# Kernel tuning notes

Hardware: AMD Instinct MI355X
Metric: run time of the kernel (lower is better)

The kernel has to match this reference:

```python
import math
import jax, jax.numpy as jnp
import numpy as np

# dims (from init_kwargs / forward signature)
B, N, K = 8, 1024, 8            # batch, nodes, num_neighbors
NC, TED, TEC = 64, 128, 64      # num_channels, time_embedding_dim, time_embedding_channels
C = NC + TEC                    # model dim = 128
H, Dh = 8, 16                   # heads, dim_head
HD = H * Dh
L = 4                           # num_layers
RH = 32                         # radial-net hidden width
NPATH = 10                      # radial scalars: k00,k10,k01,k11a,k11b,v00,v10,v01,v11a,v11b


def _g(k, shape, fan_in):
    return jax.random.normal(k, shape, dtype=jnp.float32) / np.sqrt(float(fan_in))


def setup_inputs() -> dict:
    key = jax.random.key(0)
    ks = jax.random.split(key, 16)
    return dict(
        x=jax.random.normal(ks[0], (B, N, 3), dtype=jnp.float32),
        y=jax.random.normal(ks[1], (B, N, 3), dtype=jnp.float32),
        t=jax.random.uniform(ks[2], (B,), dtype=jnp.float32) * 1000.0,
        Wt1=_g(ks[3], (TED, TED), TED), bt1=jnp.zeros((TED,), jnp.float32),
        Wt2=_g(ks[4], (TED, TEC), TED), bt2=jnp.zeros((TEC,), jnp.float32),
        Win0=_g(ks[5], (TEC + 3, C), TEC + 3), bin0=jnp.zeros((C,), jnp.float32),
        Win1=_g(ks[6], (1, C), 1),
        Wqkv=_g(ks[7], (L, 12, C, HD), C),           # q0,q1,k00,k10,k01,k11a,k11b,v00,v10,v01,v11a,v11b
        Wr1=_g(ks[8], (L, 1, RH), 1), br1=jnp.zeros((L, RH), jnp.float32),
        Wr2=_g(ks[9], (L, RH, H * NPATH), RH), br2=jnp.zeros((L, H * NPATH), jnp.float32),
        Wo=_g(ks[10], (L, 2, HD, C), HD), bo=jnp.zeros((L, 2, C), jnp.float32),
        Wout=_g(ks[11], (3, C), C), bout=jnp.zeros((3,), jnp.float32),
    )


def _forward(x, y, t, Wt1, bt1, Wt2, bt2, Win0, bin0, Win1, Wqkv,
             Wr1, br1, Wr2, br2, Wo, bo, Wout, bout):
    b, n = x.shape[0], x.shape[1]
    # sinusoidal time embedding + time MLP
    half = TED // 2
    freqs = jnp.exp(-math.log(10000.0) * jnp.arange(half, dtype=x.dtype) / half)
    emb = t[:, None] * freqs
    temb = jnp.concatenate([jnp.sin(emb), jnp.cos(emb)], axis=-1)          # [B,TED]
    temb = jax.nn.silu(temb @ Wt1 + bt1) @ Wt2 + bt2                        # [B,TEC]

    # degree-0 input = [time_embed | coords], degree-1 input = coords (1 channel)
    deg0 = jnp.concatenate([jnp.broadcast_to(temb[:, None, :], (b, n, TEC)), x], axis=-1)
    f0 = deg0 @ Win0 + bin0                                                 # [B,N,C]
    f1 = jnp.einsum('bnv,c->bncv', x, Win1[0])                              # [B,N,C,3]

    # k-nearest-neighbor graph on coordinates (shared across layers)
    d2 = jnp.sum((x[:, :, None, :] - x[:, None, :, :]) ** 2, axis=-1)       # [B,N,N]
    d2 = d2 + jnp.eye(n, dtype=x.dtype) * 1e9                               # exclude self
    _, idx = jax.lax.top_k(-d2, K)                                          # [B,N,K]
    gather = lambda f: jax.vmap(lambda a, i: a[i])(f, idx)                  # [B,N,...] -> [B,N,K,...]
    rel = gather(x) - x[:, :, None, :]                                      # [B,N,K,3]
    r = jnp.sqrt(jnp.sum(rel ** 2, axis=-1, keepdims=True) + 1e-8)          # [B,N,K,1]
    rhat = rel / r

    inv_scale = 1.0 / float(np.sqrt(2 * Dh))
    for l in range(L):
        Wl = Wqkv[l].reshape(12, C, H, Dh)
        q0 = jnp.einsum('bnc,chd->bnhd', f0, Wl[0])
        q1 = jnp.einsum('bncv,chd->bnhdv', f1, Wl[1])
        f0j, f1j = gather(f0), gather(f1)                                   # [B,N,K,C], [B,N,K,C,3]
        # radial network -> per-head, per-path scalars
        Rn = (jax.nn.silu(r @ Wr1[l] + br1[l]) @ Wr2[l] + br2[l]).reshape(b, n, K, H, NPATH)
        # equivariant tensor-product paths (degrees 0/1, spherical harmonics Y0,Y1,Y2)
        dot1 = jnp.einsum('bnkcv,bnkv->bnkc', f1j, rhat)                    # 1->0 path
        sym = 3.0 * dot1[..., None] * rhat[:, :, :, None, :] - f1j          # Y2 (traceless sym) 1->1 path
        p0 = lambda f, w: jnp.einsum('bnkc,chd->bnkhd', f, w)
        p1 = lambda f, w: jnp.einsum('bnkcv,chd->bnkhdv', f, w)
        rh = rhat[:, :, :, None, None, :]
        k0 = p0(f0j, Wl[2]) * Rn[..., 0:1] + p0(dot1, Wl[3]) * Rn[..., 1:2]
        k1 = (p0(f0j, Wl[4])[..., None] * rh * Rn[..., 2][..., None, None]
              + p1(f1j, Wl[5]) * Rn[..., 3][..., None, None]
              + p1(sym, Wl[6]) * Rn[..., 4][..., None, None])
        v0 = p0(f0j, Wl[7]) * Rn[..., 5:6] + p0(dot1, Wl[8]) * Rn[..., 6:7]
        v1 = (p0(f0j, Wl[9])[..., None] * rh * Rn[..., 7][..., None, None]
              + p1(f1j, Wl[10]) * Rn[..., 8][..., None, None]
              + p1(sym, Wl[11]) * Rn[..., 9][..., None, None])
        logits = (jnp.einsum('bnhd,bnkhd->bnhk', q0, k0)
                  + jnp.einsum('bnhdv,bnkhdv->bnhk', q1, k1)) * inv_scale
        attn = jax.nn.softmax(logits, axis=-1)
        o0 = jnp.einsum('bnhk,bnkhd->bnhd', attn, v0).reshape(b, n, HD)
        o1 = jnp.einsum('bnhk,bnkhdv->bnhdv', attn, v1).reshape(b, n, HD, 3)
        f0 = f0 + o0 @ Wo[l, 0] + bo[l, 0]
        f1 = f1 + jnp.einsum('bnev,ec->bncv', o1, Wo[l, 1]) + bo[l, 1][None, None, :, None]

    # output layer Linear(dim, 3) applied as per-component channel mixing on the type-1 output
    return jnp.einsum('bncv,vc->bnv', f1, Wout) + bout                      # [B,N,3]


def reference(x, y, t, Wt1, bt1, Wt2, bt2, Win0, bin0, Win1, Wqkv,
              Wr1, br1, Wr2, br2, Wo, bo, Wout, bout):
    return _forward(x, y, t, Wt1, bt1, Wt2, bt2, Win0, bin0, Win1, Wqkv,
                    Wr1, br1, Wr2, br2, Wo, bo, Wout, bout)
```

## Files before the change

### kernel.cpp

```cpp
#include <hip/hip_runtime.h>
#include <math.h>

#define NBATCH 8
#define NPTS   1024
#define KNN    8
#define CC     128
#define HD_    128
#define TED_   128
#define TEC_   64
#define RH     32
#define NL     4

typedef _Float16 half8 __attribute__((ext_vector_type(8)));
typedef _Float16 h4v  __attribute__((ext_vector_type(4)));
typedef float f32x4 __attribute__((ext_vector_type(4)));

__device__ __forceinline__ unsigned long long shflxor_u64(unsigned long long v, int m) {
  return (unsigned long long)__shfl_xor((long long)v, m, 8);
}

__global__ __launch_bounds__(128) void k_temb(
    const float* __restrict__ t, const float* __restrict__ Wt1,
    const float* __restrict__ bt1, const float* __restrict__ Wt2,
    const float* __restrict__ bt2, const float* __restrict__ Win0,
    const float* __restrict__ bin0, float* __restrict__ pre0)
{
  int b = blockIdx.x;
  int tid = threadIdx.x;
  __shared__ float e128[TED_];
  __shared__ float h1[TED_];
  __shared__ float te[TEC_];
  float tv = t[b];
  if (tid < 64) {
    float fr = expf((-9.210340371976184f * (float)tid) * 0.015625f);
    float em = tv * fr;
    e128[tid]      = sinf(em);
    e128[tid + 64] = cosf(em);
  }
  __syncthreads();
  {
    float acc = bt1[tid];
    for (int i = 0; i < TED_; ++i) acc += e128[i] * Wt1[i * TED_ + tid];
    h1[tid] = acc / (1.0f + expf(-acc));
  }
  __syncthreads();
  if (tid < TEC_) {
    float acc = bt2[tid];
    for (int j = 0; j < TED_; ++j) acc += h1[j] * Wt2[j * TEC_ + tid];
    te[tid] = acc;
  }
  __syncthreads();
  {
    float acc = bin0[tid];
    for (int i = 0; i < TEC_; ++i) acc += te[i] * Win0[i * CC + tid];
    pre0[b * CC + tid] = acc;
  }
}

__global__ __launch_bounds__(256) void k_init(
    const float* __restrict__ x, const float* __restrict__ Win0,
    const float* __restrict__ Win1, const float* __restrict__ pre0,
    float* __restrict__ f0, float* __restrict__ f1,
    _Float16* __restrict__ f0h, _Float16* __restrict__ f1h)
{
  int node = blockIdx.x * 2 + (threadIdx.x >> 7);
  int c = threadIdx.x & 127;
  int b = node >> 10;
  float x0 = x[node * 3 + 0], x1 = x[node * 3 + 1], x2 = x[node * 3 + 2];
  float acc = pre0[b * CC + c]
            + x0 * Win0[(TEC_ + 0) * CC + c]
            + x1 * Win0[(TEC_ + 1) * CC + c]
            + x2 * Win0[(TEC_ + 2) * CC + c];
  f0[(size_t)node * CC + c] = acc;
  f0h[(size_t)node * CC + c] = (_Float16)acc;
  float w1 = Win1[c];
  float v0 = x0 * w1, v1 = x1 * w1, v2 = x2 * w1;
  f1[((size_t)node * 3 + 0) * CC + c] = v0;
  f1[((size_t)node * 3 + 1) * CC + c] = v1;
  f1[((size_t)node * 3 + 2) * CC + c] = v2;
  f1h[((size_t)node * 3 + 0) * CC + c] = (_Float16)v0;
  f1h[((size_t)node * 3 + 1) * CC + c] = (_Float16)v1;
  f1h[((size_t)node * 3 + 2) * CC + c] = (_Float16)v2;
}

__global__ __launch_bounds__(256) void k_knn(
    const float* __restrict__ x, int* __restrict__ idx,
    float* __restrict__ rhat, float* __restrict__ rl)
{
  const int b    = blockIdx.x >> 5;
  const int tile = blockIdx.x & 31;
  const int tid  = threadIdx.x;
  const int qg   = tid >> 3;
  const int sub  = tid & 7;

  __shared__ float xsx[NPTS], xsy[NPTS], xsz[NPTS];

  for (int i = tid; i < NPTS; i += 256) {
    const float* xp = x + ((size_t)b * NPTS + i) * 3;
    xsx[i] = xp[0]; xsy[i] = xp[1]; xsz[i] = xp[2];
  }
  __syncthreads();

  const int n = tile * 32 + qg;
  const float qx = xsx[n], qy = xsy[n], qz = xsz[n];

  unsigned long long bd[KNN];
  #pragma unroll
  for (int k = 0; k < KNN; ++k) bd[k] = ~0ull;

  const int j0 = sub * 128;
  const int ph = sub * 4;
  for (int it = 0; it < 128; ++it) {
    int j = j0 + ((it + ph) & 127);
    float dx = qx - xsx[j];
    float dy = qy - xsy[j];
    float dz = qz - xsz[j];
    float s = __fadd_rn(__fadd_rn(__fmul_rn(dx, dx), __fmul_rn(dy, dy)),
                        __fmul_rn(dz, dz));
    if (j == n) s = 1.0e9f;
    unsigned long long key =
        ((unsigned long long)__float_as_uint(s) << 32) | (unsigned int)j;
    if (key < bd[KNN - 1]) {
      bd[KNN - 1] = key;
      #pragma unroll
      for (int q = KNN - 1; q > 0; --q) {
        if (bd[q] < bd[q - 1]) {
          unsigned long long tmp = bd[q]; bd[q] = bd[q - 1]; bd[q - 1] = tmp;
        }
      }
    }
  }

  unsigned long long res[KNN];
  #pragma unroll
  for (int r = 0; r < KNN; ++r) {
    unsigned long long m = bd[0];
    unsigned long long o;
    o = shflxor_u64(m, 1); m = (o < m) ? o : m;
    o = shflxor_u64(m, 2); m = (o < m) ? o : m;
    o = shflxor_u64(m, 4); m = (o < m) ? o : m;
    if (bd[0] == m) {
      #pragma unroll
      for (int q = 0; q < KNN - 1; ++q) bd[q] = bd[q + 1];
      bd[KNN - 1] = ~0ull;
    }
    res[r] = m;
  }

  unsigned long long key = res[0];
  #pragma unroll
  for (int r = 1; r < KNN; ++r) if (sub == r) key = res[r];
  int j = (int)(key & 0xffffffffu);
  size_t base = ((size_t)b * NPTS + n) * KNN + sub;
  idx[base] = j;
  float rx = xsx[j] - qx;
  float ry = xsy[j] - qy;
  float rz = xsz[j] - qz;
  float rr2 = rx * rx + ry * ry + rz * rz + 1e-8f;
  float r = sqrtf(rr2);
  rl[base] = r;
  rhat[base * 3 + 0] = rx / r;
  rhat[base * 3 + 1] = ry / r;
  rhat[base * 3 + 2] = rz / r;
}

__global__ __launch_bounds__(256) void k_rn(
    const float* __restrict__ rl, const float* __restrict__ Wr1,
    const float* __restrict__ br1, const float* __restrict__ Wr2,
    const float* __restrict__ br2, _Float16* __restrict__ Rn)
{
  const int l = blockIdx.y;
  const int e0 = blockIdx.x * 64;
  const int t = threadIdx.x;
  __shared__ _Float16 hid[64][48];
  __shared__ _Float16 wt[80][48];
  __shared__ _Float16 rn_lds[64][128];

  {
    uint4 zz = {0, 0, 0, 0};
    #pragma unroll
    for (int u = 0; u < 4; ++u)
      *(uint4*)((char*)rn_lds + (u * 256 + t) * 16) = zz;
  }
  {
    const float* wr2 = Wr2 + l * RH * 80;
    for (int i = t; i < 2560; i += 256) {
      int n = i >> 5, k = i & 31;
      wt[n][k] = (_Float16)wr2[k * 80 + n];
    }
  }
  {
    const float* wr1 = Wr1 + l * RH;
    const float* wb1 = br1 + l * RH;
    int e = t >> 2, i0 = (t & 3) * 8;
    float rv = rl[e0 + e];
    #pragma unroll
    for (int q = 0; q < 8; ++q) {
      int i = i0 + q;
      float zv = rv * wr1[i] + wb1[i];
      hid[e][i] = (_Float16)(zv / (1.0f + expf(-zv)));
    }
  }
  __syncthreads();

  {
    const int lane = t & 63;
    const int w = t >> 6;
    const int r15 = lane & 15;
    const int g = lane >> 4;
    half8 af = *(const half8*)&hid[w * 16 + r15][g * 8];
    const float* wb2 = br2 + l * 80;
    #pragma unroll
    for (int nt = 0; nt < 5; ++nt) {
      half8 bf = *(const half8*)&wt[nt * 16 + r15][g * 8];
      f32x4 acc = {};
      acc = __builtin_amdgcn_mfma_f32_16x16x32_f16(af, bf, acc, 0, 0, 0);
      int col = nt * 16 + r15;
      int hh = col / 10, j = col - hh * 10;
      float bv = wb2[col];
      #pragma unroll
      for (int i = 0; i < 4; ++i) {
        int e = w * 16 + g * 4 + i;
        rn_lds[e][hh * 16 + j] = (_Float16)(acc[i] + bv);
      }
    }
  }
  __syncthreads();
  _Float16* dst = Rn + ((size_t)l * 65536 + e0) * 128;
  #pragma unroll
  for (int u = 0; u < 4; ++u) {
    int i = u * 256 + t;
    *(uint4*)(dst + i * 8) = *(const uint4*)((const char*)rn_lds + i * 16);
  }
}

__global__ __launch_bounds__(256) void k_wconv(
    const float* __restrict__ Wqkv, const float* __restrict__ Wo,
    _Float16* __restrict__ Whq, _Float16* __restrict__ Who)
{
  __shared__ _Float16 T[128][136];
  int m = blockIdx.x;
  const float* src; _Float16* dst;
  if (m < 48) { src = Wqkv + (size_t)m * 16384; dst = Whq + (size_t)m * 16384; }
  else { src = Wo + (size_t)(m - 48) * 16384; dst = Who + (size_t)(m - 48) * 16384; }
  int tid = threadIdx.x;
  for (int i = tid; i < 16384; i += 256) {
    int k = i >> 7, n = i & 127;
    T[n][k] = (_Float16)src[i];
  }
  __syncthreads();
  for (int i = tid; i < 16384; i += 256) {
    int n = i >> 7, k = i & 127;
    dst[i] = T[n][k];
  }
}

#define MFMA_BODY(A_, ROWBASE_, WT_)                                          \
  const int tid  = threadIdx.x;                                               \
  const int lane = tid & 63;                                                  \
  const int w    = tid >> 6;                                                  \
  const int r15  = lane & 15;                                                 \
  const int g    = lane >> 4;                                                 \
  half8 bf[2][4];                                                             \
  _Pragma("unroll")                                                           \
  for (int ntl = 0; ntl < 2; ++ntl) {                                         \
    int n = (w * 2 + ntl) * 16 + r15;                                         \
    const _Float16* wp = (WT_) + (size_t)n * 128 + g * 8;                     \
    _Pragma("unroll")                                                         \
    for (int ks = 0; ks < 4; ++ks)                                            \
      bf[ntl][ks] = *(const half8*)(wp + ks * 32);                            \
  }                                                                           \
  {                                                                           \
    int r = tid >> 1;                                                         \
    const _Float16* src = (A_) + (size_t)((ROWBASE_) + r) * 128;              \
    int c0 = (tid & 1) * 8;                                                   \
    _Pragma("unroll")                                                         \
    for (int q = 0; q < 8; ++q) {                                             \
      int c = c0 + q;                                                         \
      *(uint4*)&As[r][c * 8] = *(const uint4*)(src + c * 8);                  \
    }                                                                         \
  }                                                                           \
  __syncthreads();                                                            \
  f32x4 acc[8][2] = {};                                                       \
  _Pragma("unroll")                                                           \
  for (int ks = 0; ks < 4; ++ks) {                                            \
    half8 a[8];                                                               \
    _Pragma("unroll")                                                         \
    for (int mt = 0; mt < 8; ++mt)                                            \
      a[mt] = *(const half8*)&As[mt * 16 + r15][ks * 32 + g * 8];             \
    _Pragma("unroll")                                                         \
    for (int mt = 0; mt < 8; ++mt) {                                          \
      acc[mt][0] = __builtin_amdgcn_mfma_f32_16x16x32_f16(a[mt], bf[0][ks], acc[mt][0], 0, 0, 0); \
      acc[mt][1] = __builtin_amdgcn_mfma_f32_16x16x32_f16(a[mt], bf[1][ks], acc[mt][1], 0, 0, 0); \
    }                                                                         \
  }

__global__ __launch_bounds__(256) void k_proj_mfma(
    const _Float16* __restrict__ f0h, const _Float16* __restrict__ f1h,
    const _Float16* __restrict__ Wh, _Float16* __restrict__ P0,
    _Float16* __restrict__ P1, int nb0)
{
  __shared__ _Float16 As[128][136];
  int z = blockIdx.x;
  const _Float16* A; const _Float16* Wt; _Float16* P; int ldP, colBase, rowBase;
  if (z < nb0 * 5) {
    const int map0[5] = {0, 2, 4, 7, 9};
    int m = z / nb0, rb = z - m * nb0;
    A = f0h; rowBase = rb * 128;
    Wt = Wh + (size_t)map0[m] * 16384;
    P = P0; ldP = 640; colBase = m * 128;
  } else {
    z -= nb0 * 5;
    int nb1 = nb0 * 3;
    const int map1[7] = {1, 3, 5, 6, 8, 10, 11};
    int m = z / nb1, rb = z - m * nb1;
    A = f1h; rowBase = rb * 128;
    Wt = Wh + (size_t)map1[m] * 16384;
    P = P1; ldP = 896; colBase = m * 128;
  }
  MFMA_BODY(A, rowBase, Wt)
  #pragma unroll
  for (int mt = 0; mt < 8; ++mt) {
    #pragma unroll
    for (int ntl = 0; ntl < 2; ++ntl) {
      int col = colBase + (w * 2 + ntl) * 16 + r15;
      #pragma unroll
      for (int i = 0; i < 4; ++i) {
        int r = rowBase + mt * 16 + g * 4 + i;
        P[(size_t)r * ldP + col] = (_Float16)acc[mt][ntl][i];
      }
    }
  }
}

__global__ __launch_bounds__(256) void k_wo_mfma(
    const _Float16* __restrict__ o0h, const _Float16* __restrict__ o1h,
    const _Float16* __restrict__ Who_l, const float* __restrict__ bo_l,
    float* __restrict__ f0, float* __restrict__ f1,
    _Float16* __restrict__ f0h, _Float16* __restrict__ f1h, int nb0)
{
  __shared__ _Float16 As[128][136];
  int z = blockIdx.x;
  const _Float16* A; const _Float16* Wt; const float* bias;
  float* F; _Float16* FH; int rowBase;
  if (z < nb0) {
    A = o0h; Wt = Who_l; bias = bo_l; F = f0; FH = f0h; rowBase = z * 128;
  } else {
    z -= nb0;
    A = o1h; Wt = Who_l + 16384; bias = bo_l + CC; F = f1; FH = f1h; rowBase = z * 128;
  }
  MFMA_BODY(A, rowBase, Wt)
  #pragma unroll
  for (int mt = 0; mt < 8; ++mt) {
    #pragma unroll
    for (int ntl = 0; ntl < 2; ++ntl) {
      int col = (w * 2 + ntl) * 16 + r15;
      float bv = bias[col];
      #pragma unroll
      for (int i = 0; i < 4; ++i) {
        int r = rowBase + mt * 16 + g * 4 + i;
        size_t p = (size_t)r * 128 + col;
        float val = F[p] + acc[mt][ntl][i] + bv;
        F[p] = val;
        FH[p] = (_Float16)val;
      }
    }
  }
}

__global__ __launch_bounds__(256) void k_attn(
    const _Float16* __restrict__ P0, const _Float16* __restrict__ P1,
    const int* __restrict__ idx, const float* __restrict__ rhat,
    const _Float16* __restrict__ RnL,
    _Float16* __restrict__ o0h, _Float16* __restrict__ o1h,
    int nodeBase, int nbg)
{
  const int t = threadIdx.x;
  const int wv = t >> 6;
  const int lane = t & 63;
  const int cl = lane & 31;
  const int nh = lane >> 5;
  const int z = blockIdx.x;
  const int bb = z % nbg;
  const int qbase = (z / nbg) * 4;
  const int nodeLocal = bb * NPTS + qbase + wv;
  const int node = nodeBase + nodeLocal;
  const int batchRow = bb * NPTS;

  __shared__ float rh_s[4][KNN][3];
  if (t < 96) {
    int nd = t / 24, e = t % 24;
    rh_s[nd][e / 3][e % 3] =
        rhat[((size_t)(nodeBase + bb * NPTS + qbase + nd)) * KNN * 3 + e];
  }
  __syncthreads();

  const int c0 = cl * 4;
  const int h = cl >> 2;
  const _Float16* p0n = P0 + (size_t)nodeLocal * 640 + c0;
  const _Float16* p1n = P1 + (size_t)nodeLocal * 2688 + c0;
  h4v q0v  = *(const h4v*)(p0n);
  h4v q1xv = *(const h4v*)(p1n);
  h4v q1yv = *(const h4v*)(p1n + 896);
  h4v q1zv = *(const h4v*)(p1n + 1792);

  const float inv_scale = 0.17677669529663687f;
  const int* idxp = idx + (size_t)node * KNN + nh * 4;
  int jls[4];
  #pragma unroll
  for (int k = 0; k < 4; ++k) jls[k] = batchRow + idxp[k];
  const _Float16* rnp = RnL + ((size_t)node * KNN + nh * 4) * 128 + h * 16;

  float m = -3.0e38f, ssum = 0.0f;
  float a0[4] = {}, ax[4] = {}, ay[4] = {}, az[4] = {};

  for (int k = 0; k < 4; ++k) {
    int kk = nh * 4 + k;
    int jl = jls[k];
    const _Float16* g0 = P0 + (size_t)jl * 640 + c0;
    const _Float16* g1 = P1 + (size_t)jl * 2688 + c0;
    float rx = rh_s[wv][kk][0], ry = rh_s[wv][kk][1], rz = rh_s[wv][kk][2];

    h4v G02 = *(const h4v*)(g0 + 128), G04 = *(const h4v*)(g0 + 256);
    h4v G07 = *(const h4v*)(g0 + 384), G09 = *(const h4v*)(g0 + 512);
    h4v G13x = *(const h4v*)(g1 + 128),  G13y = *(const h4v*)(g1 + 896 + 128),  G13z = *(const h4v*)(g1 + 1792 + 128);
    h4v G15x = *(const h4v*)(g1 + 256),  G15y = *(const h4v*)(g1 + 896 + 256),  G15z = *(const h4v*)(g1 + 1792 + 256);
    h4v G16x = *(const h4v*)(g1 + 384),  G16y = *(const h4v*)(g1 + 896 + 384),  G16z = *(const h4v*)(g1 + 1792 + 384);
    h4v G18x = *(const h4v*)(g1 + 512),  G18y = *(const h4v*)(g1 + 896 + 512),  G18z = *(const h4v*)(g1 + 1792 + 512);
    h4v G1Ax = *(const h4v*)(g1 + 640),  G1Ay = *(const h4v*)(g1 + 896 + 640),  G1Az = *(const h4v*)(g1 + 1792 + 640);
    h4v G1Bx = *(const h4v*)(g1 + 768),  G1By = *(const h4v*)(g1 + 896 + 768),  G1Bz = *(const h4v*)(g1 + 1792 + 768);

    half8 rv = *(const half8*)(rnp + (size_t)k * 128);
    h4v rv2 = *(const h4v*)(rnp + (size_t)k * 128 + 8);
    float r0 = (float)rv[0], r1 = (float)rv[1], r2 = (float)rv[2], r3 = (float)rv[3];
    float r4 = (float)rv[4], r5 = (float)rv[5], r6 = (float)rv[6], r7 = (float)rv[7];
    float r8 = (float)rv2[0], r9 = (float)rv2[1];

    float pl = 0.0f;
    float v0c[4], vxc[4], vyc[4], vzc[4];
    #pragma unroll
    for (int ci = 0; ci < 4; ++ci) {
      float g02 = (float)G02[ci], g04 = (float)G04[ci];
      float g07 = (float)G07[ci], g09 = (float)G09[ci];
      float g13x = (float)G13x[ci], g13y = (float)G13y[ci], g13z = (float)G13z[ci];
      float g15x = (float)G15x[ci], g15y = (float)G15y[ci], g15z = (float)G15z[ci];
      float g16x = (float)G16x[ci], g16y = (float)G16y[ci], g16z = (float)G16z[ci];
      float g18x = (float)G18x[ci], g18y = (float)G18y[ci], g18z = (float)G18z[ci];
      float g1ax = (float)G1Ax[ci], g1ay = (float)G1Ay[ci], g1az = (float)G1Az[ci];
      float g1bx = (float)G1Bx[ci], g1by = (float)G1By[ci], g1bz = (float)G1Bz[ci];

      float DP3 = g13x * rx + g13y * ry + g13z * rz;
      float DP6 = g16x * rx + g16y * ry + g16z * rz;
      float DP8 = g18x * rx + g18y * ry + g18z * rz;
      float DPB = g1bx * rx + g1by * ry + g1bz * rz;

      float k0  = g02 * r0 + DP3 * r1;
      float k1x = g04 * rx * r2 + g15x * r3 + (3.0f * rx * DP6 - g16x) * r4;
      float k1y = g04 * ry * r2 + g15y * r3 + (3.0f * ry * DP6 - g16y) * r4;
      float k1z = g04 * rz * r2 + g15z * r3 + (3.0f * rz * DP6 - g16z) * r4;
      v0c[ci] = g07 * r5 + DP8 * r6;
      vxc[ci] = g09 * rx * r7 + g1ax * r8 + (3.0f * rx * DPB - g1bx) * r9;
      vyc[ci] = g09 * ry * r7 + g1ay * r8 + (3.0f * ry * DPB - g1by) * r9;
      vzc[ci] = g09 * rz * r7 + g1az * r8 + (3.0f * rz * DPB - g1bz) * r9;

      pl += (float)q0v[ci] * k0 + (float)q1xv[ci] * k1x
          + (float)q1yv[ci] * k1y + (float)q1zv[ci] * k1z;
    }
    pl += __shfl_xor(pl, 1, 4);
    pl += __shfl_xor(pl, 2, 4);
    pl *= inv_scale;

    float mnew = fmaxf(m, pl);
    float scale = expf(m - mnew);
    float wgt = expf(pl - mnew);
    ssum = ssum * scale + wgt;
    #pragma unroll
    for (int ci = 0; ci < 4; ++ci) {
      a0[ci] = a0[ci] * scale + wgt * v0c[ci];
      ax[ci] = ax[ci] * scale + wgt * vxc[ci];
      ay[ci] = ay[ci] * scale + wgt * vyc[ci];
      az[ci] = az[ci] * scale + wgt * vzc[ci];
    }
    m = mnew;
  }

  {
    float mo = __shfl_xor(m, 32, 64);
    float so = __shfl_xor(ssum, 32, 64);
    float mn = fmaxf(m, mo);
    float s_self = expf(m - mn);
    float s_oth  = expf(mo - mn);
    ssum = ssum * s_self + so * s_oth;
    #pragma unroll
    for (int ci = 0; ci < 4; ++ci) {
      float o0 = __shfl_xor(a0[ci], 32, 64);
      float ox = __shfl_xor(ax[ci], 32, 64);
      float oy = __shfl_xor(ay[ci], 32, 64);
      float oz = __shfl_xor(az[ci], 32, 64);
      a0[ci] = a0[ci] * s_self + o0 * s_oth;
      ax[ci] = ax[ci] * s_self + ox * s_oth;
      ay[ci] = ay[ci] * s_self + oy * s_oth;
      az[ci] = az[ci] * s_self + oz * s_oth;
    }
  }

  if (nh == 0) {
    float invs = 1.0f / ssum;
    h4v o;
    #pragma unroll
    for (int ci = 0; ci < 4; ++ci) o[ci] = (_Float16)(a0[ci] * invs);
    *(h4v*)(o0h + (size_t)nodeLocal * 128 + c0) = o;
    #pragma unroll
    for (int ci = 0; ci < 4; ++ci) o[ci] = (_Float16)(ax[ci] * invs);
    *(h4v*)(o1h + ((size_t)nodeLocal * 3 + 0) * 128 + c0) = o;
    #pragma unroll
    for (int ci = 0; ci < 4; ++ci) o[ci] = (_Float16)(ay[ci] * invs);
    *(h4v*)(o1h + ((size_t)nodeLocal * 3 + 1) * 128 + c0) = o;
    #pragma unroll
    for (int ci = 0; ci < 4; ++ci) o[ci] = (_Float16)(az[ci] * invs);
    *(h4v*)(o1h + ((size_t)nodeLocal * 3 + 2) * 128 + c0) = o;
  }
}

__global__ __launch_bounds__(256) void k_out(
    const float* __restrict__ f1, const float* __restrict__ Wout,
    const float* __restrict__ bout, float* __restrict__ out)
{
  int i = blockIdx.x * 256 + threadIdx.x;
  int v = i % 3;
  const float* row = f1 + (size_t)i * CC;
  const float* w = Wout + v * CC;
  float acc = 0.0f;
  #pragma unroll
  for (int c = 0; c < CC; c += 4) {
    float4 fv = *(const float4*)&row[c];
    float4 wv = *(const float4*)&w[c];
    acc += fv.x * wv.x + fv.y * wv.y + fv.z * wv.z + fv.w * wv.w;
  }
  out[i] = acc + bout[v];
}

extern "C" void kernel_launch(void* const* d_in, const int* in_sizes, int n_in,
                              void* d_out, int out_size, void* d_ws, size_t ws_size,
                              hipStream_t stream) {
  const float* x    = (const float*)d_in[0];
  const float* t    = (const float*)d_in[2];
  const float* Wt1  = (const float*)d_in[3];
  const float* bt1  = (const float*)d_in[4];
  const float* Wt2  = (const float*)d_in[5];
  const float* bt2  = (const float*)d_in[6];
  const float* Win0 = (const float*)d_in[7];
  const float* bin0 = (const float*)d_in[8];
  const float* Win1 = (const float*)d_in[9];
  const float* Wqkv = (const float*)d_in[10];
  const float* Wr1  = (const float*)d_in[11];
  const float* br1  = (const float*)d_in[12];
  const float* Wr2  = (const float*)d_in[13];
  const float* br2  = (const float*)d_in[14];
  const float* Wo   = (const float*)d_in[15];
  const float* bo   = (const float*)d_in[16];
  const float* Wout = (const float*)d_in[17];
  const float* bout = (const float*)d_in[18];
  float* out = (float*)d_out;

  char* wsb = (char*)d_ws;
  size_t off = 0;
  auto alloc = [&](size_t bytes) -> void* {
    void* p = wsb + off;
    off = (off + bytes + 255) & ~(size_t)255;
    return p;
  };
  const int totalNodes = NBATCH * NPTS;
  float* pre0 = (float*)alloc((size_t)NBATCH * CC * 4);
  float* f0   = (float*)alloc((size_t)totalNodes * CC * 4);
  float* f1   = (float*)alloc((size_t)totalNodes * 3 * CC * 4);
  _Float16* f0h = (_Float16*)alloc((size_t)totalNodes * CC * 2);
  _Float16* f1h = (_Float16*)alloc((size_t)totalNodes * 3 * CC * 2);
  _Float16* Whq = (_Float16*)alloc((size_t)NL * 12 * CC * HD_ * 2);
  _Float16* Who = (_Float16*)alloc((size_t)NL * 2 * CC * HD_ * 2);
  int*   idx  = (int*)alloc((size_t)totalNodes * KNN * 4);
  float* rhat = (float*)alloc((size_t)totalNodes * KNN * 3 * 4);
  float* rl   = (float*)alloc((size_t)totalNodes * KNN * 4);
  _Float16* Rn = (_Float16*)alloc((size_t)NL * totalNodes * KNN * 128 * 2);
  size_t fixedBytes = off;
  size_t perBatch = (size_t)NPTS * ((640 + 2688) * 2 + (128 + 384) * 2);
  int nbg = 8;
  while (nbg > 1 && fixedBytes + (size_t)nbg * perBatch + 8192 > ws_size) nbg >>= 1;
  _Float16* P0  = (_Float16*)alloc((size_t)nbg * NPTS * 640 * 2);
  _Float16* P1  = (_Float16*)alloc((size_t)nbg * NPTS * 2688 * 2);
  _Float16* o0h = (_Float16*)alloc((size_t)nbg * NPTS * 128 * 2);
  _Float16* o1h = (_Float16*)alloc((size_t)nbg * NPTS * 384 * 2);

  k_temb<<<NBATCH, 128, 0, stream>>>(t, Wt1, bt1, Wt2, bt2, Win0, bin0, pre0);
  k_init<<<totalNodes / 2, 256, 0, stream>>>(x, Win0, Win1, pre0, f0, f1, f0h, f1h);
  k_knn<<<NBATCH * 32, 256, 0, stream>>>(x, idx, rhat, rl);
  k_wconv<<<56, 256, 0, stream>>>(Wqkv, Wo, Whq, Who);
  k_rn<<<dim3(totalNodes * KNN / 64, NL), 256, 0, stream>>>(rl, Wr1, br1, Wr2, br2, Rn);

  for (int g = 0; g < NBATCH / nbg; ++g) {
    int nodeBase = g * nbg * NPTS;
    int nodes = nbg * NPTS;
    int nb0 = nodes / 128;
    for (int l = 0; l < NL; ++l) {
      k_proj_mfma<<<nb0 * 26, 256, 0, stream>>>(
          f0h + (size_t)nodeBase * CC, f1h + (size_t)nodeBase * 3 * CC,
          Whq + (size_t)l * 12 * CC * HD_, P0, P1, nb0);
      k_attn<<<nodes / 4, 256, 0, stream>>>(
          P0, P1, idx, rhat, Rn + (size_t)l * totalNodes * KNN * 128,
          o0h, o1h, nodeBase, nbg);
      k_wo_mfma<<<nb0 * 4, 256, 0, stream>>>(
          o0h, o1h, Who + (size_t)l * 2 * CC * HD_, bo + (size_t)(l * 2) * CC,
          f0 + (size_t)nodeBase * CC, f1 + (size_t)nodeBase * 3 * CC,
          f0h + (size_t)nodeBase * CC, f1h + (size_t)nodeBase * 3 * CC, nb0);
    }
  }
  k_out<<<(totalNodes * 3) / 256, 256, 0, stream>>>(f1, Wout, bout, out);
}
```

Baseline: 416.8 us.

## Split kNN search across full wavefronts and stage attention gather loads

```diff
diff --git a/kernel.cpp b/kernel.cpp
--- a/kernel.cpp
+++ b/kernel.cpp
@@ -14,10 +14,6 @@
 typedef _Float16 half8 __attribute__((ext_vector_type(8)));
 typedef _Float16 h4v  __attribute__((ext_vector_type(4)));
 typedef float f32x4 __attribute__((ext_vector_type(4)));
-
-__device__ __forceinline__ unsigned long long shflxor_u64(unsigned long long v, int m) {
-  return (unsigned long long)__shfl_xor((long long)v, m, 8);
-}
 
 __global__ __launch_bounds__(128) void k_temb(
     const float* __restrict__ t, const float* __restrict__ Wt1,
@@ -87,11 +83,11 @@
     const float* __restrict__ x, int* __restrict__ idx,
     float* __restrict__ rhat, float* __restrict__ rl)
 {
-  const int b    = blockIdx.x >> 5;
-  const int tile = blockIdx.x & 31;
+  const int b    = blockIdx.x >> 8;
+  const int tile = blockIdx.x & 255;
   const int tid  = threadIdx.x;
-  const int qg   = tid >> 3;
-  const int sub  = tid & 7;
+  const int qg   = tid >> 6;
+  const int sub  = tid & 63;
 
   __shared__ float xsx[NPTS], xsy[NPTS], xsz[NPTS];
 
@@ -101,17 +97,17 @@
   }
   __syncthreads();
 
-  const int n = tile * 32 + qg;
+  const int n = tile * 4 + qg;
   const float qx = xsx[n], qy = xsy[n], qz = xsz[n];
 
   unsigned long long bd[KNN];
   #pragma unroll
   for (int k = 0; k < KNN; ++k) bd[k] = ~0ull;
 
-  const int j0 = sub * 128;
-  const int ph = sub * 4;
-  for (int it = 0; it < 128; ++it) {
-    int j = j0 + ((it + ph) & 127);
+  const int j0 = sub * 16;
+  #pragma unroll
+  for (int it = 0; it < 16; ++it) {
+    int j = j0 + ((it + sub) & 15);
     float dx = qx - xsx[j];
     float dy = qy - xsy[j];
     float dz = qz - xsz[j];
@@ -135,10 +131,11 @@
   #pragma unroll
   for (int r = 0; r < KNN; ++r) {
     unsigned long long m = bd[0];
-    unsigned long long o;
-    o = shflxor_u64(m, 1); m = (o < m) ? o : m;
-    o = shflxor_u64(m, 2); m = (o < m) ? o : m;
-    o = shflxor_u64(m, 4); m = (o < m) ? o : m;
+    #pragma unroll
+    for (int mk = 1; mk < 64; mk <<= 1) {
+      unsigned long long o = (unsigned long long)__shfl_xor((long long)m, mk, 64);
+      m = (o < m) ? o : m;
+    }
     if (bd[0] == m) {
       #pragma unroll
       for (int q = 0; q < KNN - 1; ++q) bd[q] = bd[q + 1];
@@ -147,21 +144,23 @@
     res[r] = m;
   }
 
-  unsigned long long key = res[0];
-  #pragma unroll
-  for (int r = 1; r < KNN; ++r) if (sub == r) key = res[r];
-  int j = (int)(key & 0xffffffffu);
-  size_t base = ((size_t)b * NPTS + n) * KNN + sub;
-  idx[base] = j;
-  float rx = xsx[j] - qx;
-  float ry = xsy[j] - qy;
-  float rz = xsz[j] - qz;
-  float rr2 = rx * rx + ry * ry + rz * rz + 1e-8f;
-  float r = sqrtf(rr2);
-  rl[base] = r;
-  rhat[base * 3 + 0] = rx / r;
-  rhat[base * 3 + 1] = ry / r;
-  rhat[base * 3 + 2] = rz / r;
+  if (sub < KNN) {
+    unsigned long long key = res[0];
+    #pragma unroll
+    for (int r = 1; r < KNN; ++r) if (sub == r) key = res[r];
+    int j = (int)(key & 0xffffffffu);
+    size_t base = ((size_t)b * NPTS + n) * KNN + sub;
+    idx[base] = j;
+    float rx = xsx[j] - qx;
+    float ry = xsy[j] - qy;
+    float rz = xsz[j] - qz;
+    float rr2 = rx * rx + ry * ry + rz * rz + 1e-8f;
+    float r = sqrtf(rr2);
+    rl[base] = r;
+    rhat[base * 3 + 0] = rx / r;
+    rhat[base * 3 + 1] = ry / r;
+    rhat[base * 3 + 2] = rz / r;
+  }
 }
 
 __global__ __launch_bounds__(256) void k_rn(
@@ -421,15 +420,6 @@
     const _Float16* g1 = P1 + (size_t)jl * 2688 + c0;
     float rx = rh_s[wv][kk][0], ry = rh_s[wv][kk][1], rz = rh_s[wv][kk][2];
 
-    h4v G02 = *(const h4v*)(g0 + 128), G04 = *(const h4v*)(g0 + 256);
-    h4v G07 = *(const h4v*)(g0 + 384), G09 = *(const h4v*)(g0 + 512);
-    h4v G13x = *(const h4v*)(g1 + 128),  G13y = *(const h4v*)(g1 + 896 + 128),  G13z = *(const h4v*)(g1 + 1792 + 128);
-    h4v G15x = *(const h4v*)(g1 + 256),  G15y = *(const h4v*)(g1 + 896 + 256),  G15z = *(const h4v*)(g1 + 1792 + 256);
-    h4v G16x = *(const h4v*)(g1 + 384),  G16y = *(const h4v*)(g1 + 896 + 384),  G16z = *(const h4v*)(g1 + 1792 + 384);
-    h4v G18x = *(const h4v*)(g1 + 512),  G18y = *(const h4v*)(g1 + 896 + 512),  G18z = *(const h4v*)(g1 + 1792 + 512);
-    h4v G1Ax = *(const h4v*)(g1 + 640),  G1Ay = *(const h4v*)(g1 + 896 + 640),  G1Az = *(const h4v*)(g1 + 1792 + 640);
-    h4v G1Bx = *(const h4v*)(g1 + 768),  G1By = *(const h4v*)(g1 + 896 + 768),  G1Bz = *(const h4v*)(g1 + 1792 + 768);
-
     half8 rv = *(const half8*)(rnp + (size_t)k * 128);
     h4v rv2 = *(const h4v*)(rnp + (size_t)k * 128 + 8);
     float r0 = (float)rv[0], r1 = (float)rv[1], r2 = (float)rv[2], r3 = (float)rv[3];
@@ -437,34 +427,26 @@
     float r8 = (float)rv2[0], r9 = (float)rv2[1];
 
     float pl = 0.0f;
-    float v0c[4], vxc[4], vyc[4], vzc[4];
-    #pragma unroll
-    for (int ci = 0; ci < 4; ++ci) {
-      float g02 = (float)G02[ci], g04 = (float)G04[ci];
-      float g07 = (float)G07[ci], g09 = (float)G09[ci];
-      float g13x = (float)G13x[ci], g13y = (float)G13y[ci], g13z = (float)G13z[ci];
-      float g15x = (float)G15x[ci], g15y = (float)G15y[ci], g15z = (float)G15z[ci];
-      float g16x = (float)G16x[ci], g16y = (float)G16y[ci], g16z = (float)G16z[ci];
-      float g18x = (float)G18x[ci], g18y = (float)G18y[ci], g18z = (float)G18z[ci];
-      float g1ax = (float)G1Ax[ci], g1ay = (float)G1Ay[ci], g1az = (float)G1Az[ci];
-      float g1bx = (float)G1Bx[ci], g1by = (float)G1By[ci], g1bz = (float)G1Bz[ci];
-
-      float DP3 = g13x * rx + g13y * ry + g13z * rz;
-      float DP6 = g16x * rx + g16y * ry + g16z * rz;
-      float DP8 = g18x * rx + g18y * ry + g18z * rz;
-      float DPB = g1bx * rx + g1by * ry + g1bz * rz;
-
-      float k0  = g02 * r0 + DP3 * r1;
-      float k1x = g04 * rx * r2 + g15x * r3 + (3.0f * rx * DP6 - g16x) * r4;
-      float k1y = g04 * ry * r2 + g15y * r3 + (3.0f * ry * DP6 - g16y) * r4;
-      float k1z = g04 * rz * r2 + g15z * r3 + (3.0f * rz * DP6 - g16z) * r4;
-      v0c[ci] = g07 * r5 + DP8 * r6;
-      vxc[ci] = g09 * rx * r7 + g1ax * r8 + (3.0f * rx * DPB - g1bx) * r9;
-      vyc[ci] = g09 * ry * r7 + g1ay * r8 + (3.0f * ry * DPB - g1by) * r9;
-      vzc[ci] = g09 * rz * r7 + g1az * r8 + (3.0f * rz * DPB - g1bz) * r9;
-
-      pl += (float)q0v[ci] * k0 + (float)q1xv[ci] * k1x
-          + (float)q1yv[ci] * k1y + (float)q1zv[ci] * k1z;
+    {
+      h4v G02 = *(const h4v*)(g0 + 128), G04 = *(const h4v*)(g0 + 256);
+      h4v G13x = *(const h4v*)(g1 + 128),  G13y = *(const h4v*)(g1 + 896 + 128),  G13z = *(const h4v*)(g1 + 1792 + 128);
+      h4v G15x = *(const h4v*)(g1 + 256),  G15y = *(const h4v*)(g1 + 896 + 256),  G15z = *(const h4v*)(g1 + 1792 + 256);
+      h4v G16x = *(const h4v*)(g1 + 384),  G16y = *(const h4v*)(g1 + 896 + 384),  G16z = *(const h4v*)(g1 + 1792 + 384);
+      #pragma unroll
+      for (int ci = 0; ci < 4; ++ci) {
+        float g02 = (float)G02[ci], g04 = (float)G04[ci];
+        float g13x = (float)G13x[ci], g13y = (float)G13y[ci], g13z = (float)G13z[ci];
+        float g15x = (float)G15x[ci], g15y = (float)G15y[ci], g15z = (float)G15z[ci];
+        float g16x = (float)G16x[ci], g16y = (float)G16y[ci], g16z = (float)G16z[ci];
+        float DP3 = g13x * rx + g13y * ry + g13z * rz;
+        float DP6 = g16x * rx + g16y * ry + g16z * rz;
+        float k0  = g02 * r0 + DP3 * r1;
+        float k1x = g04 * rx * r2 + g15x * r3 + (3.0f * rx * DP6 - g16x) * r4;
+        float k1y = g04 * ry * r2 + g15y * r3 + (3.0f * ry * DP6 - g16y) * r4;
+        float k1z = g04 * rz * r2 + g15z * r3 + (3.0f * rz * DP6 - g16z) * r4;
+        pl += (float)q0v[ci] * k0 + (float)q1xv[ci] * k1x
+            + (float)q1yv[ci] * k1y + (float)q1zv[ci] * k1z;
+      }
     }
     pl += __shfl_xor(pl, 1, 4);
     pl += __shfl_xor(pl, 2, 4);
@@ -474,14 +456,31 @@
     float scale = expf(m - mnew);
     float wgt = expf(pl - mnew);
     ssum = ssum * scale + wgt;
-    #pragma unroll
-    for (int ci = 0; ci < 4; ++ci) {
-      a0[ci] = a0[ci] * scale + wgt * v0c[ci];
-      ax[ci] = ax[ci] * scale + wgt * vxc[ci];
-      ay[ci] = ay[ci] * scale + wgt * vyc[ci];
-      az[ci] = az[ci] * scale + wgt * vzc[ci];
-    }
     m = mnew;
+
+    {
+      h4v G07 = *(const h4v*)(g0 + 384), G09 = *(const h4v*)(g0 + 512);
+      h4v G18x = *(const h4v*)(g1 + 512),  G18y = *(const h4v*)(g1 + 896 + 512),  G18z = *(const h4v*)(g1 + 1792 + 512);
+      h4v G1Ax = *(const h4v*)(g1 + 640),  G1Ay = *(const h4v*)(g1 + 896 + 640),  G1Az = *(const h4v*)(g1 + 1792 + 640);
+      h4v G1Bx = *(const h4v*)(g1 + 768),  G1By = *(const h4v*)(g1 + 896 + 768),  G1Bz = *(const h4v*)(g1 + 1792 + 768);
+      #pragma unroll
+      for (int ci = 0; ci < 4; ++ci) {
+        float g07 = (float)G07[ci], g09 = (float)G09[ci];
+        float g18x = (float)G18x[ci], g18y = (float)G18y[ci], g18z = (float)G18z[ci];
+        float g1ax = (float)G1Ax[ci], g1ay = (float)G1Ay[ci], g1az = (float)G1Az[ci];
+        float g1bx = (float)G1Bx[ci], g1by = (float)G1By[ci], g1bz = (float)G1Bz[ci];
+        float DP8 = g18x * rx + g18y * ry + g18z * rz;
+        float DPB = g1bx * rx + g1by * ry + g1bz * rz;
+        float v0  = g07 * r5 + DP8 * r6;
+        float v1x = g09 * rx * r7 + g1ax * r8 + (3.0f * rx * DPB - g1bx) * r9;
+        float v1y = g09 * ry * r7 + g1ay * r8 + (3.0f * ry * DPB - g1by) * r9;
+        float v1z = g09 * rz * r7 + g1az * r8 + (3.0f * rz * DPB - g1bz) * r9;
+        a0[ci] = a0[ci] * scale + wgt * v0;
+        ax[ci] = ax[ci] * scale + wgt * v1x;
+        ay[ci] = ay[ci] * scale + wgt * v1y;
+        az[ci] = az[ci] * scale + wgt * v1z;
+      }
+    }
   }
 
   {
@@ -593,7 +592,7 @@
 
   k_temb<<<NBATCH, 128, 0, stream>>>(t, Wt1, bt1, Wt2, bt2, Win0, bin0, pre0);
   k_init<<<totalNodes / 2, 256, 0, stream>>>(x, Win0, Win1, pre0, f0, f1, f0h, f1h);
-  k_knn<<<NBATCH * 32, 256, 0, stream>>>(x, idx, rhat, rl);
+  k_knn<<<NBATCH * 256, 256, 0, stream>>>(x, idx, rhat, rl);
   k_wconv<<<56, 256, 0, stream>>>(Wqkv, Wo, Whq, Who);
   k_rn<<<dim3(totalNodes * KNN / 64, NL), 256, 0, stream>>>(rl, Wr1, br1, Wr2, br2, Rn);
 
```

After: 376.2 us, median of 2. -9.7%, faster.
